# Kernel optimization log

Hardware: AMD Instinct MI355X
Metric: run time of the kernel (lower is better)

The kernel has to match this reference:

```python
import jax, jax.numpy as jnp
import numpy as np

U, I, D = 100000, 50000, 64
N = U + I
E_G, E_U, E_I = 2400000, 1600000, 800000


def _spmm(rows, cols, vals, x, n):
    # sparse [n, m] @ dense [m, d] via gather + scale + segment-sum scatter
    return jax.ops.segment_sum(x[cols] * vals[:, None], rows, num_segments=n)


def setup_inputs() -> dict:
    key = jax.random.key(0)
    ks = jax.random.split(key, 11)
    return {
        "user_emb": jax.random.normal(ks[0], (U, D), dtype=jnp.float32),
        "item_emb": jax.random.normal(ks[1], (I, D), dtype=jnp.float32),
        "graph_rows": jax.random.randint(ks[2], (E_G,), 0, N, dtype=jnp.int32),
        "graph_cols": jax.random.randint(ks[3], (E_G,), 0, N, dtype=jnp.int32),
        "graph_vals": jax.random.uniform(ks[4], (E_G,), dtype=jnp.float32),
        "user_rows": jax.random.randint(ks[5], (E_U,), 0, U, dtype=jnp.int32),
        "user_cols": jax.random.randint(ks[6], (E_U,), 0, U, dtype=jnp.int32),
        "user_vals": jax.random.uniform(ks[7], (E_U,), dtype=jnp.float32),
        "item_rows": jax.random.randint(ks[8], (E_I,), 0, I, dtype=jnp.int32),
        "item_cols": jax.random.randint(ks[9], (E_I,), 0, I, dtype=jnp.int32),
        "item_vals": jax.random.uniform(ks[10], (E_I,), dtype=jnp.float32),
    }


def reference(user_emb, item_emb,
              graph_rows, graph_cols, graph_vals,
              user_rows, user_cols, user_vals,
              item_rows, item_cols, item_vals):
    all_emb = jnp.concatenate([user_emb, item_emb], axis=0)  # [N, D]
    all_emb1 = _spmm(graph_rows, graph_cols, graph_vals, all_emb, N)
    user_emb2 = _spmm(user_rows, user_cols, user_vals, user_emb, U)
    item_emb2 = _spmm(item_rows, item_cols, item_vals, item_emb, I)
    user_emb1, item_emb1 = all_emb1[:U], all_emb1[U:]
    return (user_emb1, item_emb1, user_emb2, item_emb2)
```

## Files before the change

kernel.cpp:

```cpp
#include <hip/hip_runtime.h>

#define DDIM 64
constexpr int U_CNT = 100000;
constexpr int I_CNT = 50000;
constexpr int N_CNT = U_CNT + I_CNT;
constexpr int NB    = N_CNT + U_CNT + I_CNT;

constexpr int BIN_ROWS_LOG = 7;
constexpr int BIN_ROWS = 1 << BIN_ROWS_LOG;
constexpr int BINS = (NB + BIN_ROWS - 1) / BIN_ROWS;
constexpr int BINS_PAD = 2560;
constexpr int SORT_EDGES = 4096;
constexpr int HIST_EDGES = 16384;
constexpr int CAP = 2432;
constexpr int NSLOT = 10;

constexpr int SB_LOG = 12;
constexpr int NSB = (NB + (1 << SB_LOG) - 1) >> SB_LOG;
constexpr int NSB_PAD = 128;
constexpr int BWIN = 80;
constexpr int BWIN_PAD = 128;

typedef unsigned u32x2 __attribute__((ext_vector_type(2)));
typedef unsigned u32x4 __attribute__((ext_vector_type(4)));
typedef float    f32x2 __attribute__((ext_vector_type(2)));

__device__ __forceinline__ int wave_incl_scan(int v, int lane) {
#pragma unroll
    for (int off = 1; off < 64; off <<= 1) {
        int t = __shfl_up(v, off, 64);
        if (lane >= off) v += t;
    }
    return v;
}

__device__ __forceinline__ unsigned short f2bf_rne(float f) {
    unsigned u = __float_as_uint(f);
    unsigned r = (u + 0x7FFFu + ((u >> 16) & 1u)) >> 16;
    return (unsigned short)r;
}

__global__ __launch_bounds__(256) void convert_emb(const float* __restrict__ ue,
                                                   const float* __restrict__ ie,
                                                   unsigned short* __restrict__ emb16) {
    int g = blockIdx.x * 256 + threadIdx.x;
    constexpr int UG = U_CNT * (DDIM / 4);
    constexpr int TG = N_CNT * (DDIM / 4);
    if (g >= TG) return;
    float4 v = (g < UG) ? ((const float4*)ue)[g] : ((const float4*)ie)[g - UG];
    ushort4 o;
    o.x = f2bf_rne(v.x); o.y = f2bf_rne(v.y); o.z = f2bf_rne(v.z); o.w = f2bf_rne(v.w);
    ((ushort4*)emb16)[g] = o;
}

__global__ __launch_bounds__(1024) void hist_conv(const int* __restrict__ gr,
                                                  const int* __restrict__ ur,
                                                  const int* __restrict__ ir,
                                                  int EG, int EU, int EI,
                                                  int* __restrict__ cnt,
                                                  const float* __restrict__ ue,
                                                  const float* __restrict__ ie,
                                                  unsigned short* __restrict__ emb16) {
    __shared__ int h[BINS_PAD];
    for (int i = threadIdx.x; i < BINS_PAD; i += 1024) h[i] = 0;

    if (emb16) {
        constexpr int UG = U_CNT * (DDIM / 4);
        constexpr int TG = N_CNT * (DDIM / 4);
        int stride = (int)gridDim.x * 1024;
        for (int g = blockIdx.x * 1024 + threadIdx.x; g < TG; g += stride) {
            float4 v = (g < UG) ? ((const float4*)ue)[g] : ((const float4*)ie)[g - UG];
            ushort4 o;
            o.x = f2bf_rne(v.x); o.y = f2bf_rne(v.y); o.z = f2bf_rne(v.z); o.w = f2bf_rne(v.w);
            ((ushort4*)emb16)[g] = o;
        }
    }
    __syncthreads();

    int base = blockIdx.x * HIST_EDGES;
    int Et = EG + EU + EI;
    for (int j = 0; j < HIST_EDGES / 1024; ++j) {
        int e = base + j * 1024 + threadIdx.x;
        if (e < Et) {
            int b;
            if (e < EG)           b = gr[e];
            else if (e < EG + EU) b = N_CNT + ur[e - EG];
            else                  b = N_CNT + U_CNT + ir[e - EG - EU];
            atomicAdd(&h[b >> BIN_ROWS_LOG], 1);
        }
    }
    __syncthreads();
    for (int i = threadIdx.x; i < BINS; i += 1024) {
        int v = h[i];
        if (v) atomicAdd(&cnt[i], v);
    }
}

__global__ __launch_bounds__(1024) void scan_bins(const int* __restrict__ cnt,
                                                  int* __restrict__ bin_base,
                                                  int* __restrict__ bin_cursor,
                                                  int* __restrict__ sb_base,
                                                  int* __restrict__ sb_cursor,
                                                  int E_total) {
    __shared__ int wsum[16], woff[16];
    int tid = threadIdx.x, lane = tid & 63, wid = tid >> 6;
    int i0 = 3 * tid, i1 = i0 + 1, i2 = i0 + 2;
    int c0 = (i0 < BINS) ? cnt[i0] : 0;
    int c1 = (i1 < BINS) ? cnt[i1] : 0;
    int c2 = (i2 < BINS) ? cnt[i2] : 0;
    int v = c0 + c1 + c2;
    int incl = wave_incl_scan(v, lane);
    if (lane == 63) wsum[wid] = incl;
    __syncthreads();
    if (wid == 0 && lane < 16) {
        int s = wsum[lane], si = s;
#pragma unroll
        for (int off = 1; off < 16; off <<= 1) {
            int t = __shfl_up(si, off, 64);
            if (lane >= off) si += t;
        }
        woff[lane] = si - s;
    }
    __syncthreads();
    int e = incl - v + woff[wid];
    if (i0 < BINS) { bin_base[i0] = e;           bin_cursor[i0] = e; }
    if (i1 < BINS) { bin_base[i1] = e + c0;      bin_cursor[i1] = e + c0; }
    if (i2 < BINS) { bin_base[i2] = e + c0 + c1; bin_cursor[i2] = e + c0 + c1; }
    if (tid == 0) bin_base[BINS] = E_total;
    __syncthreads();
    if (tid <= NSB) {
        int idx = tid << (SB_LOG - BIN_ROWS_LOG);
        int vv = (idx >= BINS) ? E_total : bin_base[idx];
        sb_base[tid] = vv;
        if (tid < NSB) sb_cursor[tid] = vv;
    }
}

__global__ __launch_bounds__(512, 8) void sbsort_all(
        const int* __restrict__ gr, const int* __restrict__ gc, const float* __restrict__ gv,
        const int* __restrict__ ur, const int* __restrict__ uc, const float* __restrict__ uv,
        const int* __restrict__ ir, const int* __restrict__ ic, const float* __restrict__ iv,
        int EG, int EU, int EI,
        int* __restrict__ sb_cursor, uint2* __restrict__ poolA) {
    __shared__ uint2 sorted[SORT_EDGES];
    __shared__ unsigned char ssb[SORT_EDGES];
    __shared__ int hist[NSB_PAD];
    __shared__ int lscan[NSB_PAD];
    __shared__ int lcur[NSB_PAD];
    __shared__ int wsum2[2];

    int tid = threadIdx.x, lane = tid & 63, wid = tid >> 6;
    for (int i = tid; i < NSB_PAD; i += 512) { hist[i] = 0; lcur[i] = 0; }
    __syncthreads();

    const int Et = EG + EU + EI;
    int start = blockIdx.x * SORT_EDGES;
    int base_e = start + tid * 8;
    int myb[8]; unsigned mylo[8]; float myv[8];

#pragma unroll
    for (int j = 0; j < 8; j += 4) {
        int e = base_e + j;
        int sg0 = (e < EG) ? 0 : (e < EG + EU ? 1 : 2);
        int sg3 = (e + 3 < EG) ? 0 : (e + 3 < EG + EU ? 1 : 2);
        if (e + 3 < Et && sg0 == sg3) {
            const int* R; const int* Cc; const float* V; int boff, goff, loc;
            if (sg0 == 0)      { R = gr; Cc = gc; V = gv; boff = 0;             goff = 0;     loc = e; }
            else if (sg0 == 1) { R = ur; Cc = uc; V = uv; boff = N_CNT;         goff = 0;     loc = e - EG; }
            else               { R = ir; Cc = ic; V = iv; boff = N_CNT + U_CNT; goff = U_CNT; loc = e - EG - EU; }
            int4   r4 = *(const int4*)(R + loc);
            int4   c4 = *(const int4*)(Cc + loc);
            float4 v4 = *(const float4*)(V + loc);
            int rr[4] = {r4.x, r4.y, r4.z, r4.w};
            int cc[4] = {c4.x, c4.y, c4.z, c4.w};
            float vv[4] = {v4.x, v4.y, v4.z, v4.w};
#pragma unroll
            for (int q = 0; q < 4; ++q) {
                int bucket = boff + rr[q];
                int sb = bucket >> SB_LOG;
                myb[j + q] = sb;
                mylo[j + q] = ((unsigned)(bucket & 4095) << 18) | (unsigned)(goff + cc[q]);
                myv[j + q] = vv[q];
                atomicAdd(&hist[sb], 1);
            }
        } else {
#pragma unroll
            for (int q = 0; q < 4; ++q) {
                int ee = e + q;
                if (ee < Et) {
                    int r, c; float vl; int boff, goff;
                    if (ee < EG)           { r = gr[ee]; c = gc[ee]; vl = gv[ee]; boff = 0; goff = 0; }
                    else if (ee < EG + EU) { int k = ee - EG;      r = ur[k]; c = uc[k]; vl = uv[k]; boff = N_CNT;         goff = 0; }
                    else                   { int k = ee - EG - EU; r = ir[k]; c = ic[k]; vl = iv[k]; boff = N_CNT + U_CNT; goff = U_CNT; }
                    int bucket = boff + r;
                    int sb = bucket >> SB_LOG;
                    myb[j + q] = sb;
                    mylo[j + q] = ((unsigned)(bucket & 4095) << 18) | (unsigned)(goff + c);
                    myv[j + q] = vl;
                    atomicAdd(&hist[sb], 1);
                } else myb[j + q] = -1;
            }
        }
    }
    __syncthreads();

    int v = 0, incl = 0;
    if (tid < NSB_PAD) {
        v = hist[tid];
        incl = wave_incl_scan(v, lane);
        if (lane == 63) wsum2[wid] = incl;
    }
    __syncthreads();
    if (tid < NSB_PAD) {
        int st = incl - v + (wid ? wsum2[0] : 0);
        lscan[tid] = st;
        if (tid < NSB && v) hist[tid] = atomicAdd(&sb_cursor[tid], v);
    }
    __syncthreads();

#pragma unroll
    for (int j = 0; j < 8; ++j) {
        if (myb[j] >= 0) {
            int p = lscan[myb[j]] + atomicAdd(&lcur[myb[j]], 1);
            sorted[p] = make_uint2(mylo[j], __float_as_uint(myv[j]));
            ssb[p] = (unsigned char)myb[j];
        }
    }
    __syncthreads();

    int cntE = min(SORT_EDGES, Et - start);
    for (int pos = tid; pos < cntE; pos += 512) {
        int b = ssb[pos];
        uint2 t = sorted[pos];
        u32x2 q; q.x = t.x; q.y = t.y;
        __builtin_nontemporal_store(q, (u32x2*)&poolA[hist[b] + (pos - lscan[b])]);
    }
}

__global__ __launch_bounds__(512, 8) void binsort2(const uint2* __restrict__ poolA,
                                                   const int* __restrict__ sb_base, int Et,
                                                   int* __restrict__ bin_cursor,
                                                   uint2* __restrict__ poolB) {
    __shared__ uint2 sorted[SORT_EDGES];
    __shared__ unsigned char sbin[SORT_EDGES];
    __shared__ int hist[BWIN_PAD];
    __shared__ int lscan[BWIN_PAD];
    __shared__ int lcur[BWIN_PAD];
    __shared__ int ssbb[NSB + 1];
    __shared__ int wsum2[2];
    __shared__ int sblo_s, nloc;

    int tid = threadIdx.x, lane = tid & 63, wid = tid >> 6;
    if (tid < BWIN_PAD) hist[tid] = 0;
    if (tid <= NSB) ssbb[tid] = sb_base[tid];
    __syncthreads();

    int start = blockIdx.x * SORT_EDGES;
    int base_e = start + tid * 8;
    int sb;
    {
        int lo2 = 0, hi2 = NSB - 1;
        while (lo2 < hi2) {
            int mid = (lo2 + hi2 + 1) >> 1;
            if (ssbb[mid] <= base_e) lo2 = mid; else hi2 = mid - 1;
        }
        sb = lo2;
    }
    if (tid == 0) {
        int lo2 = 0, hi2 = NSB - 1;
        while (lo2 < hi2) {
            int mid = (lo2 + hi2 + 1) >> 1;
            if (ssbb[mid] <= start) lo2 = mid; else hi2 = mid - 1;
        }
        sblo_s = lo2;
    }
    __syncthreads();
    int sb_lo = sblo_s;
    int W0 = sb_lo << (SB_LOG - BIN_ROWS_LOG);

    int myb[8]; uint2 myp[8];
#pragma unroll
    for (int j = 0; j < 8; j += 2) {
        int e = base_e + j;
        uint2 p0, p1;
        bool v1 = (e + 1 < Et), v0 = (e < Et);
        if (v1) {
            u32x4 q = __builtin_nontemporal_load((const u32x4*)(poolA + e));
            p0.x = q.x; p0.y = q.y; p1.x = q.z; p1.y = q.w;
        } else if (v0) {
            u32x2 q = __builtin_nontemporal_load((const u32x2*)(poolA + e));
            p0.x = q.x; p0.y = q.y;
        }
        if (v0) {
            while (sb < NSB - 1 && e >= ssbb[sb + 1]) ++sb;
            int slot = ((sb - sb_lo) << (SB_LOG - BIN_ROWS_LOG)) + (int)(p0.x >> 25);
            if ((unsigned)slot < (unsigned)BWIN) {
                myb[j] = slot; myp[j] = p0;
                atomicAdd(&hist[slot], 1);
            } else {
                int b = (sb << (SB_LOG - BIN_ROWS_LOG)) + (int)(p0.x >> 25);
                int gp = atomicAdd(&bin_cursor[b], 1);
                poolB[gp] = p0;
                myb[j] = -1;
            }
        } else myb[j] = -1;
        if (v1) {
            int e1 = e + 1;
            while (sb < NSB - 1 && e1 >= ssbb[sb + 1]) ++sb;
            int slot = ((sb - sb_lo) << (SB_LOG - BIN_ROWS_LOG)) + (int)(p1.x >> 25);
            if ((unsigned)slot < (unsigned)BWIN) {
                myb[j + 1] = slot; myp[j + 1] = p1;
                atomicAdd(&hist[slot], 1);
            } else {
                int b = (sb << (SB_LOG - BIN_ROWS_LOG)) + (int)(p1.x >> 25);
                int gp = atomicAdd(&bin_cursor[b], 1);
                poolB[gp] = p1;
                myb[j + 1] = -1;
            }
        } else myb[j + 1] = -1;
    }
    __syncthreads();

    int v = 0, incl = 0;
    if (tid < BWIN_PAD) {
        v = hist[tid];
        incl = wave_incl_scan(v, lane);
        if (lane == 63) wsum2[wid] = incl;
    }
    __syncthreads();
    if (tid < BWIN_PAD) {
        int st = incl - v + (wid ? wsum2[0] : 0);
        lscan[tid] = st; lcur[tid] = st;
        if (tid == BWIN_PAD - 1) nloc = st + v;
    }
    __syncthreads();
    if (tid < BWIN && hist[tid] > 0)
        hist[tid] = atomicAdd(&bin_cursor[W0 + tid], hist[tid]);
    __syncthreads();

#pragma unroll
    for (int j = 0; j < 8; ++j) {
        if (myb[j] >= 0) {
            int p = atomicAdd(&lcur[myb[j]], 1);
            sorted[p] = myp[j];
            sbin[p] = (unsigned char)myb[j];
        }
    }
    __syncthreads();

    int tot = nloc;
    for (int pos = tid; pos < tot; pos += 512) {
        int sl = sbin[pos];
        uint2 t = sorted[pos];
        u32x2 q; q.x = t.x; q.y = t.y;
        __builtin_nontemporal_store(q, (u32x2*)&poolB[hist[sl] + (pos - lscan[sl])]);
    }
}

__global__ __launch_bounds__(256, 7) void refine_accum(const int* __restrict__ bin_base,
                                                       const uint2* __restrict__ pool,
                                                       const unsigned short* __restrict__ emb16,
                                                       float* __restrict__ out) {
    __shared__ uint2 sorted[CAP + 1];
    __shared__ int rhist[BIN_ROWS];
    __shared__ int rstart[BIN_ROWS];
    __shared__ int rcur[BIN_ROWS];
    __shared__ int wsum[2];
    int tid = threadIdx.x, lane = tid & 63, wid = tid >> 6;
    int b = blockIdx.x;
    int s = bin_base[b], e = bin_base[b + 1];
    int cnt = min(e - s, CAP);

    if (tid < BIN_ROWS) rhist[tid] = 0;
    __syncthreads();

    uint2 my[NSLOT];
    const u32x2* poolv = (const u32x2*)(pool + s);
#pragma unroll
    for (int j = 0; j < NSLOT; ++j) {
        int idx = tid + j * 256;
        if (idx < cnt) {
            u32x2 q = __builtin_nontemporal_load(poolv + idx);
            my[j].x = q.x; my[j].y = q.y;
            atomicAdd(&rhist[(q.x >> 18) & 127u], 1);
        }
    }
    __syncthreads();

    int v = 0, incl = 0;
    if (tid < BIN_ROWS) {
        v = rhist[tid];
        incl = wave_incl_scan(v, lane);
        if (lane == 63) wsum[wid] = incl;
    }
    __syncthreads();
    if (tid < BIN_ROWS) {
        int st = incl - v + (wid ? wsum[0] : 0);
        rstart[tid] = st; rcur[tid] = st;
    }
    __syncthreads();

#pragma unroll
    for (int j = 0; j < NSLOT; ++j) {
        int idx = tid + j * 256;
        if (idx < cnt) {
            int pos = atomicAdd(&rcur[(my[j].x >> 18) & 127u], 1);
            sorted[pos] = my[j];
        }
    }
    if (tid == 0) sorted[cnt] = make_uint2(0u, 0u);
    __syncthreads();

    long long rowbase = (long long)b * BIN_ROWS;
    int half = lane >> 5, hl = lane & 31;
    const unsigned* emb32 = (const unsigned*)emb16;
    for (int r = wid; r < BIN_ROWS; r += 4) {
        long long row = rowbase + r;
        if (row >= NB) break;
        int k = rstart[r], ke = k + rhist[r];
        float a0 = 0.f, a1 = 0.f, c0 = 0.f, c1 = 0.f;
        for (; k + 8 <= ke; k += 8) {
            uint2 p0 = sorted[k + half];
            uint2 p1 = sorted[k + 2 + half];
            uint2 p2 = sorted[k + 4 + half];
            uint2 p3 = sorted[k + 6 + half];
            unsigned w0 = emb32[((size_t)(p0.x & 0x3FFFFu) << 5) + hl];
            unsigned w1 = emb32[((size_t)(p1.x & 0x3FFFFu) << 5) + hl];
            unsigned w2 = emb32[((size_t)(p2.x & 0x3FFFFu) << 5) + hl];
            unsigned w3 = emb32[((size_t)(p3.x & 0x3FFFFu) << 5) + hl];
            float v0 = __uint_as_float(p0.y), v1 = __uint_as_float(p1.y);
            float v2 = __uint_as_float(p2.y), v3 = __uint_as_float(p3.y);
            a0 += v0 * __uint_as_float(w0 << 16);
            a1 += v0 * __uint_as_float(w0 & 0xFFFF0000u);
            c0 += v1 * __uint_as_float(w1 << 16);
            c1 += v1 * __uint_as_float(w1 & 0xFFFF0000u);
            a0 += v2 * __uint_as_float(w2 << 16);
            a1 += v2 * __uint_as_float(w2 & 0xFFFF0000u);
            c0 += v3 * __uint_as_float(w3 << 16);
            c1 += v3 * __uint_as_float(w3 & 0xFFFF0000u);
        }
        for (; k + 2 <= ke; k += 2) {
            uint2 p = sorted[k + half];
            unsigned w = emb32[((size_t)(p.x & 0x3FFFFu) << 5) + hl];
            float v = __uint_as_float(p.y);
            a0 += v * __uint_as_float(w << 16);
            a1 += v * __uint_as_float(w & 0xFFFF0000u);
        }
        if (k < ke) {
            uint2 p = sorted[k + half];
            unsigned w = emb32[((size_t)(p.x & 0x3FFFFu) << 5) + hl];
            float v = half ? 0.f : __uint_as_float(p.y);
            a0 += v * __uint_as_float(w << 16);
            a1 += v * __uint_as_float(w & 0xFFFF0000u);
        }
        a0 += c0; a1 += c1;
        a0 += __shfl_xor(a0, 32, 64);
        a1 += __shfl_xor(a1, 32, 64);
        if (lane < 32) {
            f32x2 o; o.x = a0; o.y = a1;
            __builtin_nontemporal_store(o, (f32x2*)(out + (size_t)row * DDIM + 2 * hl));
        }
    }
}

__global__ void spmm_graph_kernel(const int* __restrict__ rows, const int* __restrict__ cols,
                                  const float* __restrict__ vals,
                                  const float* __restrict__ user_emb,
                                  const float* __restrict__ item_emb,
                                  float* __restrict__ out, int E) {
    long long idx = (long long)blockIdx.x * blockDim.x + threadIdx.x;
    int e = (int)(idx >> 6), d = (int)(idx & 63);
    if (e >= E) return;
    int r = rows[e], c = cols[e];
    float v = vals[e];
    float x = (c < U_CNT) ? user_emb[(long long)c * DDIM + d]
                          : item_emb[(long long)(c - U_CNT) * DDIM + d];
    atomicAdd(&out[(long long)r * DDIM + d], v * x);
}

__global__ void spmm_plain_kernel(const int* __restrict__ rows, const int* __restrict__ cols,
                                  const float* __restrict__ vals,
                                  const float* __restrict__ emb,
                                  float* __restrict__ out, int E) {
    long long idx = (long long)blockIdx.x * blockDim.x + threadIdx.x;
    int e = (int)(idx >> 6), d = (int)(idx & 63);
    if (e >= E) return;
    int r = rows[e], c = cols[e];
    atomicAdd(&out[(long long)r * DDIM + d], vals[e] * emb[(long long)c * DDIM + d]);
}

extern "C" void kernel_launch(void* const* d_in, const int* in_sizes, int n_in,
                              void* d_out, int out_size, void* d_ws, size_t ws_size,
                              hipStream_t stream) {
    const float* user_emb = (const float*)d_in[0];
    const float* item_emb = (const float*)d_in[1];
    const int*   g_rows   = (const int*)d_in[2];
    const int*   g_cols   = (const int*)d_in[3];
    const float* g_vals   = (const float*)d_in[4];
    const int*   u_rows   = (const int*)d_in[5];
    const int*   u_cols   = (const int*)d_in[6];
    const float* u_vals   = (const float*)d_in[7];
    const int*   i_rows   = (const int*)d_in[8];
    const int*   i_cols   = (const int*)d_in[9];
    const float* i_vals   = (const float*)d_in[10];
    float* out = (float*)d_out;

    const int EG = in_sizes[2];
    const int EU = in_sizes[5];
    const int EI = in_sizes[8];
    const int Et = EG + EU + EI;

    const size_t emb_bytes = (size_t)N_CNT * DDIM * sizeof(unsigned short);

    size_t t_off_bb   = (size_t)BINS_PAD * sizeof(int);
    size_t t_off_bc   = t_off_bb + (size_t)(BINS + 1) * sizeof(int);
    size_t t_off_sbb  = t_off_bc + (size_t)BINS * sizeof(int);
    size_t t_off_sbc  = t_off_sbb + (size_t)(NSB + 1) * sizeof(int);
    size_t t_off_pa   = (t_off_sbc + (size_t)NSB * sizeof(int) + 127) & ~(size_t)127;
    size_t t_off_pb   = (t_off_pa + (size_t)Et * sizeof(uint2) + 127) & ~(size_t)127;
    size_t needed_2p  = t_off_pb + (size_t)Et * sizeof(uint2);
    size_t t_off_emb  = (needed_2p + 127) & ~(size_t)127;
    size_t needed_na  = t_off_emb + emb_bytes;
    bool pa_fits_emb  = (size_t)Et * sizeof(uint2) >= emb_bytes;

    if (ws_size >= needed_2p && pa_fits_emb) {
        bool noalias = (ws_size >= needed_na);
        int*   cnt        = (int*)d_ws;
        int*   bin_base   = (int*)((char*)d_ws + t_off_bb);
        int*   bin_cursor = (int*)((char*)d_ws + t_off_bc);
        int*   sb_base    = (int*)((char*)d_ws + t_off_sbb);
        int*   sb_cursor  = (int*)((char*)d_ws + t_off_sbc);
        uint2* poolA      = (uint2*)((char*)d_ws + t_off_pa);
        uint2* poolB      = (uint2*)((char*)d_ws + t_off_pb);
        unsigned short* emb16 = noalias ? (unsigned short*)((char*)d_ws + t_off_emb)
                                        : (unsigned short*)poolA;

        hipMemsetAsync(cnt, 0, (size_t)BINS_PAD * sizeof(int), stream);

        unsigned hblocks = (unsigned)((Et + HIST_EDGES - 1) / HIST_EDGES);
        hist_conv<<<hblocks, 1024, 0, stream>>>(g_rows, u_rows, i_rows, EG, EU, EI, cnt,
                                                user_emb, item_emb,
                                                noalias ? emb16 : (unsigned short*)nullptr);
        scan_bins<<<1, 1024, 0, stream>>>(cnt, bin_base, bin_cursor, sb_base, sb_cursor, Et);

        unsigned nb2 = (unsigned)((Et + SORT_EDGES - 1) / SORT_EDGES);
        sbsort_all<<<nb2, 512, 0, stream>>>(g_rows, g_cols, g_vals,
                                            u_rows, u_cols, u_vals,
                                            i_rows, i_cols, i_vals,
                                            EG, EU, EI, sb_cursor, poolA);
        binsort2<<<nb2, 512, 0, stream>>>(poolA, sb_base, Et, bin_cursor, poolB);

        if (!noalias) {
            unsigned cgrid = (unsigned)((N_CNT * (DDIM / 4) + 255) / 256);
            convert_emb<<<cgrid, 256, 0, stream>>>(user_emb, item_emb, emb16);
        }

        refine_accum<<<BINS, 256, 0, stream>>>(bin_base, poolB, emb16, out);
    } else {
        hipMemsetAsync(d_out, 0, (size_t)out_size * sizeof(float), stream);
        const int block = 256;
        {
            long long t = (long long)EG * DDIM;
            spmm_graph_kernel<<<(unsigned)((t + block - 1) / block), block, 0, stream>>>(
                g_rows, g_cols, g_vals, user_emb, item_emb, out, EG);
        }
        {
            long long t = (long long)EU * DDIM;
            spmm_plain_kernel<<<(unsigned)((t + block - 1) / block), block, 0, stream>>>(
                u_rows, u_cols, u_vals, user_emb, out + (size_t)N_CNT * DDIM, EU);
        }
        {
            long long t = (long long)EI * DDIM;
            spmm_plain_kernel<<<(unsigned)((t + block - 1) / block), block, 0, stream>>>(
                i_rows, i_cols, i_vals, item_emb, out + (size_t)(N_CNT + U_CNT) * DDIM, EI);
        }
    }
}
```

Before: 355.4 us.

## Widen refine_accum blocks to 512 threads and split tail bins across two blocks

refine_accum now runs 512-thread blocks with 8 waves walking the rows of a bin. Bins past index RSPLIT are handled by two blocks, each owning 64 of the 128 rows, so the grid grows and the tail of the launch is balanced. Each split block still loads the whole bin's edge list and drops the edges outside its row range. That redundant pool traffic, plus the extra barrier and sentinel logic, is the price for more parallelism and a lighter per-block tail.

Measured after the change: 325.0 us. 1.09x faster.

```diff
diff --git a/kernel.cpp b/kernel.cpp
--- a/kernel.cpp
+++ b/kernel.cpp
@@ -13,7 +13,8 @@
 constexpr int SORT_EDGES = 4096;
 constexpr int HIST_EDGES = 16384;
 constexpr int CAP = 2432;
-constexpr int NSLOT = 10;
+constexpr int NSLOT = 5;
+constexpr int RSPLIT = 2048;
 
 constexpr int SB_LOG = 12;
 constexpr int NSB = (NB + (1 << SB_LOG) - 1) >> SB_LOG;
@@ -357,7 +358,7 @@
     }
 }
 
-__global__ __launch_bounds__(256, 7) void refine_accum(const int* __restrict__ bin_base,
+__global__ __launch_bounds__(512, 8) void refine_accum(const int* __restrict__ bin_base,
                                                        const uint2* __restrict__ pool,
                                                        const unsigned short* __restrict__ emb16,
                                                        float* __restrict__ out) {
@@ -367,7 +368,16 @@
     __shared__ int rcur[BIN_ROWS];
     __shared__ int wsum[2];
     int tid = threadIdx.x, lane = tid & 63, wid = tid >> 6;
-    int b = blockIdx.x;
+
+    int b, rlo, rhi;
+    if ((int)blockIdx.x < RSPLIT) {
+        b = blockIdx.x; rlo = 0; rhi = BIN_ROWS;
+    } else {
+        int ix = (int)blockIdx.x - RSPLIT;
+        b = RSPLIT + (ix >> 1);
+        rlo = (ix & 1) << 6;
+        rhi = rlo + 64;
+    }
     int s = bin_base[b], e = bin_base[b + 1];
     int cnt = min(e - s, CAP);
 
@@ -378,11 +388,12 @@
     const u32x2* poolv = (const u32x2*)(pool + s);
 #pragma unroll
     for (int j = 0; j < NSLOT; ++j) {
-        int idx = tid + j * 256;
+        int idx = tid + j * 512;
         if (idx < cnt) {
             u32x2 q = __builtin_nontemporal_load(poolv + idx);
             my[j].x = q.x; my[j].y = q.y;
-            atomicAdd(&rhist[(q.x >> 18) & 127u], 1);
+            int rl = (int)((q.x >> 18) & 127u);
+            if (rl >= rlo && rl < rhi) atomicAdd(&rhist[rl], 1);
         }
     }
     __syncthreads();
@@ -402,19 +413,26 @@
 
 #pragma unroll
     for (int j = 0; j < NSLOT; ++j) {
-        int idx = tid + j * 256;
+        int idx = tid + j * 512;
         if (idx < cnt) {
-            int pos = atomicAdd(&rcur[(my[j].x >> 18) & 127u], 1);
-            sorted[pos] = my[j];
-        }
-    }
-    if (tid == 0) sorted[cnt] = make_uint2(0u, 0u);
+            int rl = (int)((my[j].x >> 18) & 127u);
+            if (rl >= rlo && rl < rhi) {
+                int pos = atomicAdd(&rcur[rl], 1);
+                sorted[pos] = my[j];
+            }
+        }
+    }
+    __syncthreads();
+    if (tid == 0) {
+        int total = rcur[rhi - 1];
+        sorted[total] = make_uint2(0u, 0u);
+    }
     __syncthreads();
 
     long long rowbase = (long long)b * BIN_ROWS;
     int half = lane >> 5, hl = lane & 31;
     const unsigned* emb32 = (const unsigned*)emb16;
-    for (int r = wid; r < BIN_ROWS; r += 4) {
+    for (int r = rlo + wid; r < rhi; r += 8) {
         long long row = rowbase + r;
         if (row >= NB) break;
         int k = rstart[r], ke = k + rhist[r];
@@ -555,7 +573,8 @@
             convert_emb<<<cgrid, 256, 0, stream>>>(user_emb, item_emb, emb16);
         }
 
-        refine_accum<<<BINS, 256, 0, stream>>>(bin_base, poolB, emb16, out);
+        unsigned rgrid = (unsigned)(RSPLIT + 2 * (BINS - RSPLIT));
+        refine_accum<<<rgrid, 512, 0, stream>>>(bin_base, poolB, emb16, out);
     } else {
         hipMemsetAsync(d_out, 0, (size_t)out_size * sizeof(float), stream);
         const int block = 256;
```
